# Kernel tuning notes

Measured on AMD Instinct MI355X. Metric: run time of the kernel, lower is better.

## Reference

```python
import jax, jax.numpy as jnp
import numpy as np

B, L, P, A, D = 64, 512, 64, 16, 512  # batch, seq_len, n_positions, n_actions, n_lstm


def setup_inputs() -> dict:
    key = jax.random.key(0)
    ks = jax.random.split(key, 6)
    F = P + A
    observations = jax.random.normal(ks[0], (B, L, P), jnp.float32)
    actions = jax.random.normal(ks[1], (B, L, A), jnp.float32)
    # xavier_normal init as in the torch module
    W_ci = jax.random.normal(ks[2], (F, D), jnp.float32) * np.float32(np.sqrt(2.0 / (F + D)))
    b_ci = jnp.zeros((D,), jnp.float32)
    R_ig = jax.random.normal(ks[3], (D, D), jnp.float32) * np.float32(np.sqrt(2.0 / (D + D)))
    b_ig = jnp.zeros((D,), jnp.float32)
    W_out = jax.random.normal(ks[4], (D, 1), jnp.float32) * np.float32(np.sqrt(2.0 / (D + 1)))
    b_out = jnp.zeros((1,), jnp.float32)
    return dict(observations=observations, actions=actions, W_ci=W_ci, b_ci=b_ci,
                R_ig=R_ig, b_ig=b_ig, W_out=W_out, b_out=b_out)


def reference(observations, actions, W_ci, b_ci, R_ig, b_ig, W_out, b_out):
    # Custom LSTM: forget gate = 1, output gate = 1, a_out = identity =>
    #   h_t = c_t = c_{t-1} + tanh(x_t @ W_ci + b_ci) * sigmoid(h_{t-1} @ R_ig + b_ig)
    x = jnp.concatenate([observations, actions], axis=-1)          # [B, L, F]
    ci = jnp.tanh(jnp.einsum('blf,fd->bld', x, W_ci) + b_ci)       # precompute cell input [B, L, D]
    ci_seq = jnp.swapaxes(ci, 0, 1)                                # [L, B, D] for scan
    h0 = jnp.zeros((x.shape[0], R_ig.shape[0]), x.dtype)

    def step(h, ci_t):
        ig = jax.nn.sigmoid(h @ R_ig + b_ig)
        h_new = h + ci_t * ig
        return h_new, h_new

    _, hs = jax.lax.scan(step, h0, ci_seq)                         # hs: [L, B, D]
    hs = jnp.swapaxes(hs, 0, 1)                                    # [B, L, D]
    return hs @ W_out + b_out                                      # [B, L, 1]
```

## Files before the change

### kernel.cpp

```cpp
#include <hip/hip_runtime.h>


#define B_  64
#define L_  512
#define P_  64
#define A_  16
#define D_  512
#define F_  80
#define CI_R 8

#define CI_BYTES   ((size_t)B_ * L_ * D_ * 2)
#define RP_BYTES   ((size_t)D_ * D_ * 2)
#define HBUF_UINTS (2 * B_ * 2 * 256)
#define PBANK      ((size_t)B_ * 2 * 256)
#define BATCH_CAP  4096

typedef _Float16 half2_t __attribute__((ext_vector_type(2)));
typedef unsigned int uintx4 __attribute__((ext_vector_type(4)));

__device__ __forceinline__ float dot2(unsigned int r, unsigned int h, float acc) {
    return __builtin_amdgcn_fdot2(__builtin_bit_cast(half2_t, h),
                                  __builtin_bit_cast(half2_t, r), acc, false);
}
__device__ __forceinline__ float dot4u(uintx4 r, uintx4 h, float acc) {
    acc = dot2(r.x, h.x, acc);
    acc = dot2(r.y, h.y, acc);
    acc = dot2(r.z, h.z, acc);
    acc = dot2(r.w, h.w, acc);
    return acc;
}
template<int CTRL>
__device__ __forceinline__ float dpp_mov(float v) {
    return __builtin_bit_cast(float, __builtin_amdgcn_update_dpp(
        0, __builtin_bit_cast(int, v), CTRL, 0xF, 0xF, true));
}

__device__ __forceinline__ unsigned int pk_f16(float a, float b) {
    return __builtin_bit_cast(unsigned int, __builtin_amdgcn_cvt_pkrtz(a, b));
}
__device__ __forceinline__ unsigned int ld_sc01(const unsigned int* p) {
    unsigned int v;
    asm volatile("global_load_dword %0, %1, off sc0 sc1\n\t"
                 "s_waitcnt vmcnt(0)" : "=v"(v) : "v"(p) : "memory");
    return v;
}
__device__ __forceinline__ void at_swap(unsigned int* p, unsigned int v) {
    asm volatile("global_atomic_swap %0, %1, off sc1" :: "v"(p), "v"(v) : "memory");
}
__device__ __forceinline__ int swz4(int i) {
    return ((i >> 3) << 3) | ((i + (i >> 3)) & 7);
}

__global__ __launch_bounds__(256) void prep_kernel(const float* __restrict__ R,
        unsigned int* __restrict__ Rp, unsigned int* __restrict__ hbuf,
        float* __restrict__ out) {
    int id = blockIdx.x * 256 + threadIdx.x;
    int dw = id & 3;
    int U = id >> 2;
    int tid_s = U & 511;
    int m  = (U >> 9) & 31;
    int qq = U >> 14;
    int w = tid_s >> 6, l = tid_s & 63, r = l >> 3, g = l & 7;
    int hh = m >> 4, j = (m >> 2) & 3, c = m & 3;
    int d  = qq * 256 + (w * 8 + r) * 4 + j;
    int k0 = hh * 256 + (g & 3) * 64 + (g >> 2) * 32 + c * 8 + 2 * dw;
    half2_t v;
    v.x = (_Float16)R[k0 * D_ + d];
    v.y = (_Float16)R[(k0 + 1) * D_ + d];
    Rp[id] = __builtin_bit_cast(unsigned int, v);
    if (id < HBUF_UINTS) hbuf[id] = 0u;
    if (id < B_ * L_) out[id] = 0.f;
}

__global__ __launch_bounds__(256) void ci_kernel(const float* __restrict__ obs,
                                                 const float* __restrict__ act,
                                                 const float* __restrict__ W,
                                                 const float* __restrict__ bci,
                                                 unsigned short* __restrict__ ci) {
    __shared__ float xs[CI_R][F_];
    int row0 = blockIdx.x * CI_R;
    int tid = threadIdx.x;
    for (int idx = tid; idx < CI_R * F_; idx += 256) {
        int r = idx / F_, f = idx % F_;
        float v = (f < P_) ? obs[(size_t)(row0 + r) * P_ + f]
                           : act[(size_t)(row0 + r) * A_ + (f - P_)];
        xs[r][f] = v;
    }
    __syncthreads();
    int d0 = tid, d1 = tid + 256;
    float a0[CI_R], a1[CI_R];
    #pragma unroll
    for (int r = 0; r < CI_R; ++r) { a0[r] = 0.f; a1[r] = 0.f; }
    for (int f = 0; f < F_; ++f) {
        float w0 = W[f * D_ + d0];
        float w1 = W[f * D_ + d1];
        #pragma unroll
        for (int r = 0; r < CI_R; ++r) {
            float xv = xs[r][f];
            a0[r] += xv * w0;
            a1[r] += xv * w1;
        }
    }
    float b0 = bci[d0], b1 = bci[d1];
    #pragma unroll
    for (int r = 0; r < CI_R; ++r) {
        float z0 = a0[r] + b0, z1 = a1[r] + b1;
        float e0 = __expf(-2.f * __builtin_fabsf(z0));
        float e1 = __expf(-2.f * __builtin_fabsf(z1));
        float m0 = (1.f - e0) * __builtin_amdgcn_rcpf(1.f + e0);
        float m1 = (1.f - e1) * __builtin_amdgcn_rcpf(1.f + e1);
        float t0 = z0 < 0.f ? -m0 : m0;
        float t1 = z1 < 0.f ? -m1 : m1;
        ci[(size_t)(row0 + r) * D_ + d0] = __builtin_bit_cast(unsigned short, (_Float16)t0);
        ci[(size_t)(row0 + r) * D_ + d1] = __builtin_bit_cast(unsigned short, (_Float16)t1);
    }
}

__global__ __launch_bounds__(512, 2)
__attribute__((amdgpu_waves_per_eu(2, 2)))
void scan_kernel(const unsigned int* __restrict__ Rp,
                 const unsigned short* __restrict__ ci,
                 const float* __restrict__ b_ig, const float* __restrict__ W_out,
                 const float* __restrict__ b_out, float* __restrict__ out,
                 unsigned int* __restrict__ hbuf)
{
    const int tid = threadIdx.x;
    const int bid = blockIdx.x;
    const int row = bid & 63;
    const int q   = bid >> 6;
    const int w = tid >> 6;
    const int l = tid & 63;
    const int r = l >> 3;
    const int g = l & 7;
    const int g3 = g & 3;

    __shared__ __align__(16) unsigned int hp2[128];
    __shared__ __align__(16) unsigned int hst[128];

    const uintx4* tb = (const uintx4*)Rp + (size_t)q * 16384 + tid;
    const int qx = q << 4;
    uintx4 rr[32];
    #pragma unroll
    for (int mm = 0; mm < 32; ++mm) rr[mm] = tb[(mm ^ qx) * 512];
    #pragma unroll
    for (int mm = 0; mm < 32; ++mm) asm volatile("" : "+v"(rr[mm]));

    const int dloc = (w * 8 + r) * 4 + g3;
    const int down = q * 256 + dloc;
    const float bg = b_ig[down];
    const float wo = W_out[down];
    const float bo = b_out[0];
    const unsigned short* cip = ci + (size_t)row * L_ * D_ + down;

    const int u_own = (w * 8 + r) * 2 + (g >> 1);
    const int wslot = swz4(u_own >> 2) * 4 + (u_own & 3);
    const int s_f = tid & 255;
    const int stslot = swz4(s_f >> 3) * 4 + ((s_f >> 1) & 3);
    const int ib = (g & 3) * 8 + (g >> 2) * 4;
    const int ri0 = swz4(ib + 0), ri1 = swz4(ib + 1);
    const int ri2 = swz4(ib + 2), ri3 = swz4(ib + 3);

    const unsigned int* rdbase = hbuf + ((size_t)row * 2 + (1 - q)) * 256 + s_f;
    unsigned int* wrbase = hbuf + ((size_t)row * 2 + q) * 256 + dloc;

    float hval = 0.f;
    __syncthreads();

    #pragma unroll 1
    for (int t = 0; t < L_; ++t) {
        unsigned short cu = cip[(size_t)t * D_];

        unsigned int vfetch = 0;
        const unsigned int* src = rdbase + (size_t)((t - 1) & 1) * PBANK;
        if (t > 0 && tid < 256) {
            asm volatile("global_load_dword %0, %1, off sc0 sc1"
                         : "=&v"(vfetch) : "v"(src) : "memory");
        }

        float p0 = 0.f, p1 = 0.f, p2 = 0.f, p3 = 0.f;

        if (t > 0) {
            const uintx4* hp4 = (const uintx4*)hp2;
            uintx4 h0 = hp4[ri0], h1 = hp4[ri1], h2 = hp4[ri2], h3 = hp4[ri3];
            p0 = dot4u(rr[0],  h0, p0); p0 = dot4u(rr[1],  h1, p0);
            p0 = dot4u(rr[2],  h2, p0); p0 = dot4u(rr[3],  h3, p0);
            p1 = dot4u(rr[4],  h0, p1); p1 = dot4u(rr[5],  h1, p1);
            p1 = dot4u(rr[6],  h2, p1); p1 = dot4u(rr[7],  h3, p1);
            p2 = dot4u(rr[8],  h0, p2); p2 = dot4u(rr[9],  h1, p2);
            p2 = dot4u(rr[10], h2, p2); p2 = dot4u(rr[11], h3, p2);
            p3 = dot4u(rr[12], h0, p3); p3 = dot4u(rr[13], h1, p3);
            p3 = dot4u(rr[14], h2, p3); p3 = dot4u(rr[15], h3, p3);
        }

        if (t > 0 && tid < 256) {
            asm volatile("s_waitcnt vmcnt(0)" : "+v"(vfetch) :: "memory");
            const unsigned int tt = (unsigned int)t;
            if ((vfetch & 0xffffu) != tt) {
                int it = 0;
                unsigned int a0, a1, a2;
                for (;;) {
                    asm volatile("global_load_dword %0, %1, off sc0 sc1"
                                 : "=&v"(a0) : "v"(src) : "memory");
                    __builtin_amdgcn_s_sleep(1);
                    asm volatile("global_load_dword %0, %1, off sc0 sc1"
                                 : "=&v"(a1) : "v"(src) : "memory");
                    __builtin_amdgcn_s_sleep(1);
                    asm volatile("global_load_dword %0, %1, off sc0 sc1"
                                 : "=&v"(a2) : "v"(src) : "memory");
                    asm volatile("s_waitcnt vmcnt(2)" ::: "memory");
                    if ((a0 & 0xffffu) == tt) {
                        vfetch = a0;
                        asm volatile("s_waitcnt vmcnt(0)" ::: "memory");
                        break;
                    }
                    asm volatile("s_waitcnt vmcnt(1)" ::: "memory");
                    if ((a1 & 0xffffu) == tt) {
                        vfetch = a1;
                        asm volatile("s_waitcnt vmcnt(0)" ::: "memory");
                        break;
                    }
                    asm volatile("s_waitcnt vmcnt(0)" ::: "memory");
                    if ((a2 & 0xffffu) == tt) { vfetch = a2; break; }
                    if (++it > BATCH_CAP) break;
                    __builtin_amdgcn_s_sleep(1);
                }
            }
            unsigned int vo = __builtin_bit_cast(unsigned int,
                                dpp_mov<0xB1>(__builtin_bit_cast(float, vfetch)));
            if ((tid & 1) == 0)
                hst[stslot] = (vfetch >> 16) | (vo & 0xffff0000u);
        }

        asm volatile("s_waitcnt lgkmcnt(0)" ::: "memory");
        __builtin_amdgcn_s_barrier();
        asm volatile("" ::: "memory");

        if (t > 0) {
            const uintx4* hs4 = (const uintx4*)hst;
            uintx4 h0 = hs4[ri0], h1 = hs4[ri1], h2 = hs4[ri2], h3 = hs4[ri3];
            p0 = dot4u(rr[16], h0, p0); p0 = dot4u(rr[17], h1, p0);
            p0 = dot4u(rr[18], h2, p0); p0 = dot4u(rr[19], h3, p0);
            p1 = dot4u(rr[20], h0, p1); p1 = dot4u(rr[21], h1, p1);
            p1 = dot4u(rr[22], h2, p1); p1 = dot4u(rr[23], h3, p1);
            p2 = dot4u(rr[24], h0, p2); p2 = dot4u(rr[25], h1, p2);
            p2 = dot4u(rr[26], h2, p2); p2 = dot4u(rr[27], h3, p2);
            p3 = dot4u(rr[28], h0, p3); p3 = dot4u(rr[29], h1, p3);
            p3 = dot4u(rr[30], h2, p3); p3 = dot4u(rr[31], h3, p3);
        }

        float s0 = p0 + dpp_mov<0x141>(p0);
        float s1 = p1 + dpp_mov<0x141>(p1);
        float s2 = p2 + dpp_mov<0x141>(p2);
        float s3 = p3 + dpp_mov<0x141>(p3);
        s0 = s0 + dpp_mov<0xB1>(s0);  s1 = s1 + dpp_mov<0xB1>(s1);
        s2 = s2 + dpp_mov<0xB1>(s2);  s3 = s3 + dpp_mov<0xB1>(s3);
        s0 = s0 + dpp_mov<0x4E>(s0);  s1 = s1 + dpp_mov<0x4E>(s1);
        s2 = s2 + dpp_mov<0x4E>(s2);  s3 = s3 + dpp_mov<0x4E>(s3);
        float z = ((g3 & 2) ? ((g3 & 1) ? s3 : s2)
                            : ((g3 & 1) ? s1 : s0)) + bg;

        float ig  = __builtin_amdgcn_rcpf(1.f + __expf(-z));
        float civ = (float)__builtin_bit_cast(_Float16, cu);
        hval += civ * ig;

        if (g < 4) {
            unsigned int hb = pk_f16(hval, hval) & 0xffffu;
            at_swap(wrbase + (size_t)(t & 1) * PBANK,
                    (hb << 16) | (unsigned int)(t + 1));
        }

        float nbh = dpp_mov<0xB1>(hval);
        if (g == 0 || g == 2) {
            hp2[wslot] = pk_f16(hval, nbh);
        }

        asm volatile("s_waitcnt lgkmcnt(0)" ::: "memory");
        __builtin_amdgcn_s_barrier();
        asm volatile("" ::: "memory");

        float po = (g < 4) ? hval * wo : 0.f;
        po += dpp_mov<0xB1>(po);
        po += dpp_mov<0x4E>(po);
        po += dpp_mov<0x141>(po);
        po += dpp_mov<0x140>(po);
        po += dpp_mov<0x142>(po);
        po += dpp_mov<0x143>(po);
        if (l == 63) {
            float addv = po + ((q == 0 && w == 0) ? bo : 0.f);
            atomicAdd(out + row * L_ + t, addv);
        }
    }
}

extern "C" void kernel_launch(void* const* d_in, const int* in_sizes, int n_in,
                              void* d_out, int out_size, void* d_ws, size_t ws_size,
                              hipStream_t stream) {
    const float* obs   = (const float*)d_in[0];
    const float* act   = (const float*)d_in[1];
    const float* W_ci  = (const float*)d_in[2];
    const float* b_ci  = (const float*)d_in[3];
    const float* R_ig  = (const float*)d_in[4];
    const float* b_ig  = (const float*)d_in[5];
    const float* W_out = (const float*)d_in[6];
    const float* b_out = (const float*)d_in[7];
    float* out = (float*)d_out;

    unsigned short* ci = (unsigned short*)d_ws;
    unsigned int* Rp   = (unsigned int*)((char*)d_ws + CI_BYTES);
    unsigned int* hbuf = (unsigned int*)((char*)d_ws + CI_BYTES + RP_BYTES);

    prep_kernel<<<512, 256, 0, stream>>>(R_ig, Rp, hbuf, out);
    ci_kernel<<<(B_ * L_) / CI_R, 256, 0, stream>>>(obs, act, W_ci, b_ci, ci);
    scan_kernel<<<B_ * 2, 512, 0, stream>>>(Rp, ci, b_ig, W_out, b_out, out, hbuf);
}
```

Measured before the change: 641.8 us.

## Fuse cell-input projection into scan kernel and drop separate ci kernel

Removes the standalone ci_kernel and its 32MB fp16 cell-input buffer. The prep kernel now packs W_ci and the concatenated inputs into fp16 pairs, and the scan kernel computes tanh(x·W_ci+b) per step with fdot2, using W_ci held in registers. This saves a kernel launch and the HBM round trip of the ci tensor. In exchange, the serial recurrence loop gains a 40-term dot product plus ten 16-byte loads per step, which may lengthen the critical path and raise register pressure.

```diff
diff --git a/kernel.cpp b/kernel.cpp
--- a/kernel.cpp
+++ b/kernel.cpp
@@ -7,10 +7,12 @@
 #define A_  16
 #define D_  512
 #define F_  80
-#define CI_R 8
-
-#define CI_BYTES   ((size_t)B_ * L_ * D_ * 2)
+
+#define XP_UINTS   (B_ * L_ * 40)
+#define XP_BYTES   ((size_t)XP_UINTS * 4)
 #define RP_BYTES   ((size_t)D_ * D_ * 2)
+#define WP_UINTS   (2 * 512 * 40)
+#define WP_BYTES   ((size_t)WP_UINTS * 4)
 #define HBUF_UINTS (2 * B_ * 2 * 256)
 #define PBANK      ((size_t)B_ * 2 * 256)
 #define BATCH_CAP  4096
@@ -38,12 +40,6 @@
 __device__ __forceinline__ unsigned int pk_f16(float a, float b) {
     return __builtin_bit_cast(unsigned int, __builtin_amdgcn_cvt_pkrtz(a, b));
 }
-__device__ __forceinline__ unsigned int ld_sc01(const unsigned int* p) {
-    unsigned int v;
-    asm volatile("global_load_dword %0, %1, off sc0 sc1\n\t"
-                 "s_waitcnt vmcnt(0)" : "=v"(v) : "v"(p) : "memory");
-    return v;
-}
 __device__ __forceinline__ void at_swap(unsigned int* p, unsigned int v) {
     asm volatile("global_atomic_swap %0, %1, off sc1" :: "v"(p), "v"(v) : "memory");
 }
@@ -52,74 +48,60 @@
 }
 
 __global__ __launch_bounds__(256) void prep_kernel(const float* __restrict__ R,
-        unsigned int* __restrict__ Rp, unsigned int* __restrict__ hbuf,
-        float* __restrict__ out) {
-    int id = blockIdx.x * 256 + threadIdx.x;
-    int dw = id & 3;
-    int U = id >> 2;
-    int tid_s = U & 511;
-    int m  = (U >> 9) & 31;
-    int qq = U >> 14;
-    int w = tid_s >> 6, l = tid_s & 63, r = l >> 3, g = l & 7;
-    int hh = m >> 4, j = (m >> 2) & 3, c = m & 3;
-    int d  = qq * 256 + (w * 8 + r) * 4 + j;
-    int k0 = hh * 256 + (g & 3) * 64 + (g >> 2) * 32 + c * 8 + 2 * dw;
-    half2_t v;
-    v.x = (_Float16)R[k0 * D_ + d];
-    v.y = (_Float16)R[(k0 + 1) * D_ + d];
-    Rp[id] = __builtin_bit_cast(unsigned int, v);
-    if (id < HBUF_UINTS) hbuf[id] = 0u;
-    if (id < B_ * L_) out[id] = 0.f;
-}
-
-__global__ __launch_bounds__(256) void ci_kernel(const float* __restrict__ obs,
-                                                 const float* __restrict__ act,
-                                                 const float* __restrict__ W,
-                                                 const float* __restrict__ bci,
-                                                 unsigned short* __restrict__ ci) {
-    __shared__ float xs[CI_R][F_];
-    int row0 = blockIdx.x * CI_R;
-    int tid = threadIdx.x;
-    for (int idx = tid; idx < CI_R * F_; idx += 256) {
-        int r = idx / F_, f = idx % F_;
-        float v = (f < P_) ? obs[(size_t)(row0 + r) * P_ + f]
-                           : act[(size_t)(row0 + r) * A_ + (f - P_)];
-        xs[r][f] = v;
-    }
-    __syncthreads();
-    int d0 = tid, d1 = tid + 256;
-    float a0[CI_R], a1[CI_R];
-    #pragma unroll
-    for (int r = 0; r < CI_R; ++r) { a0[r] = 0.f; a1[r] = 0.f; }
-    for (int f = 0; f < F_; ++f) {
-        float w0 = W[f * D_ + d0];
-        float w1 = W[f * D_ + d1];
-        #pragma unroll
-        for (int r = 0; r < CI_R; ++r) {
-            float xv = xs[r][f];
-            a0[r] += xv * w0;
-            a1[r] += xv * w1;
-        }
-    }
-    float b0 = bci[d0], b1 = bci[d1];
-    #pragma unroll
-    for (int r = 0; r < CI_R; ++r) {
-        float z0 = a0[r] + b0, z1 = a1[r] + b1;
-        float e0 = __expf(-2.f * __builtin_fabsf(z0));
-        float e1 = __expf(-2.f * __builtin_fabsf(z1));
-        float m0 = (1.f - e0) * __builtin_amdgcn_rcpf(1.f + e0);
-        float m1 = (1.f - e1) * __builtin_amdgcn_rcpf(1.f + e1);
-        float t0 = z0 < 0.f ? -m0 : m0;
-        float t1 = z1 < 0.f ? -m1 : m1;
-        ci[(size_t)(row0 + r) * D_ + d0] = __builtin_bit_cast(unsigned short, (_Float16)t0);
-        ci[(size_t)(row0 + r) * D_ + d1] = __builtin_bit_cast(unsigned short, (_Float16)t1);
+        const float* __restrict__ Wci, const float* __restrict__ obs,
+        const float* __restrict__ act, unsigned int* __restrict__ Rp,
+        unsigned int* __restrict__ Wp, unsigned int* __restrict__ xp,
+        unsigned int* __restrict__ hbuf, float* __restrict__ out) {
+    int blk = blockIdx.x;
+    if (blk < 512) {
+        int id = blk * 256 + threadIdx.x;
+        int dw = id & 3;
+        int U = id >> 2;
+        int tid_s = U & 511;
+        int m  = (U >> 9) & 31;
+        int qq = U >> 14;
+        int w = tid_s >> 6, l = tid_s & 63, r = l >> 3, g = l & 7;
+        int hh = m >> 4, j = (m >> 2) & 3, c = m & 3;
+        int d  = qq * 256 + (w * 8 + r) * 4 + j;
+        int k0 = hh * 256 + (g & 3) * 64 + (g >> 2) * 32 + c * 8 + 2 * dw;
+        half2_t v;
+        v.x = (_Float16)R[k0 * D_ + d];
+        v.y = (_Float16)R[(k0 + 1) * D_ + d];
+        Rp[id] = __builtin_bit_cast(unsigned int, v);
+        if (id < WP_UINTS) {
+            int i2 = id % 40, u2 = id / 40;
+            int q2 = u2 >> 9, t2 = u2 & 511;
+            int w2 = t2 >> 6, l2 = t2 & 63, r2 = l2 >> 3, g2 = l2 & 7;
+            int down2 = q2 * 256 + (w2 * 8 + r2) * 4 + (g2 & 3);
+            Wp[id] = pk_f16(Wci[(2 * i2) * D_ + down2],
+                            Wci[(2 * i2 + 1) * D_ + down2]);
+        }
+        if (id < HBUF_UINTS) hbuf[id] = 0u;
+        if (id < B_ * L_) out[id] = 0.f;
+    } else {
+        int id = (blk - 512) * 256 + threadIdx.x;
+        if (id < XP_UINTS) {
+            int i = id % 40, u = id / 40;
+            int t = u & 511, row = u >> 9;
+            float x0, x1;
+            if (i < 32) {
+                const float* ob = obs + ((size_t)row * L_ + t) * P_;
+                x0 = ob[2 * i]; x1 = ob[2 * i + 1];
+            } else {
+                const float* ac = act + ((size_t)row * L_ + t) * A_;
+                x0 = ac[2 * (i - 32)]; x1 = ac[2 * (i - 32) + 1];
+            }
+            xp[id] = pk_f16(x0, x1);
+        }
     }
 }
 
 __global__ __launch_bounds__(512, 2)
 __attribute__((amdgpu_waves_per_eu(2, 2)))
 void scan_kernel(const unsigned int* __restrict__ Rp,
-                 const unsigned short* __restrict__ ci,
+                 const unsigned int* __restrict__ Wp,
+                 const unsigned int* __restrict__ xp,
+                 const float* __restrict__ b_ci,
                  const float* __restrict__ b_ig, const float* __restrict__ W_out,
                  const float* __restrict__ b_out, float* __restrict__ out,
                  unsigned int* __restrict__ hbuf)
@@ -150,7 +132,16 @@
     const float bg = b_ig[down];
     const float wo = W_out[down];
     const float bo = b_out[0];
-    const unsigned short* cip = ci + (size_t)row * L_ * D_ + down;
+    const float bci = b_ci[down];
+
+    const uintx4* wpt = (const uintx4*)(Wp + ((size_t)q * 512 + tid) * 40);
+    uintx4 wv[10];
+    #pragma unroll
+    for (int i = 0; i < 10; ++i) wv[i] = wpt[i];
+    #pragma unroll
+    for (int i = 0; i < 10; ++i) asm volatile("" : "+v"(wv[i]));
+
+    const uintx4* xpt = (const uintx4*)(xp + (size_t)row * L_ * 40);
 
     const int u_own = (w * 8 + r) * 2 + (g >> 1);
     const int wslot = swz4(u_own >> 2) * 4 + (u_own & 3);
@@ -168,7 +159,11 @@
 
     #pragma unroll 1
     for (int t = 0; t < L_; ++t) {
-        unsigned short cu = cip[(size_t)t * D_];
+        uintx4 xv0 = xpt[t * 10 + 0], xv1 = xpt[t * 10 + 1];
+        uintx4 xv2 = xpt[t * 10 + 2], xv3 = xpt[t * 10 + 3];
+        uintx4 xv4 = xpt[t * 10 + 4], xv5 = xpt[t * 10 + 5];
+        uintx4 xv6 = xpt[t * 10 + 6], xv7 = xpt[t * 10 + 7];
+        uintx4 xv8 = xpt[t * 10 + 8], xv9 = xpt[t * 10 + 9];
 
         unsigned int vfetch = 0;
         const unsigned int* src = rdbase + (size_t)((t - 1) & 1) * PBANK;
@@ -191,6 +186,16 @@
             p3 = dot4u(rr[12], h0, p3); p3 = dot4u(rr[13], h1, p3);
             p3 = dot4u(rr[14], h2, p3); p3 = dot4u(rr[15], h3, p3);
         }
+
+        float zci = bci;
+        zci = dot4u(wv[0], xv0, zci); zci = dot4u(wv[1], xv1, zci);
+        zci = dot4u(wv[2], xv2, zci); zci = dot4u(wv[3], xv3, zci);
+        zci = dot4u(wv[4], xv4, zci); zci = dot4u(wv[5], xv5, zci);
+        zci = dot4u(wv[6], xv6, zci); zci = dot4u(wv[7], xv7, zci);
+        zci = dot4u(wv[8], xv8, zci); zci = dot4u(wv[9], xv9, zci);
+        float eci = __expf(-2.f * __builtin_fabsf(zci));
+        float mci = (1.f - eci) * __builtin_amdgcn_rcpf(1.f + eci);
+        float civ = zci < 0.f ? -mci : mci;
 
         if (t > 0 && tid < 256) {
             asm volatile("s_waitcnt vmcnt(0)" : "+v"(vfetch) :: "memory");
@@ -259,8 +264,7 @@
         float z = ((g3 & 2) ? ((g3 & 1) ? s3 : s2)
                             : ((g3 & 1) ? s1 : s0)) + bg;
 
-        float ig  = __builtin_amdgcn_rcpf(1.f + __expf(-z));
-        float civ = (float)__builtin_bit_cast(_Float16, cu);
+        float ig = __builtin_amdgcn_rcpf(1.f + __expf(-z));
         hval += civ * ig;
 
         if (g < 4) {
@@ -305,11 +309,12 @@
     const float* b_out = (const float*)d_in[7];
     float* out = (float*)d_out;
 
-    unsigned short* ci = (unsigned short*)d_ws;
-    unsigned int* Rp   = (unsigned int*)((char*)d_ws + CI_BYTES);
-    unsigned int* hbuf = (unsigned int*)((char*)d_ws + CI_BYTES + RP_BYTES);
-
-    prep_kernel<<<512, 256, 0, stream>>>(R_ig, Rp, hbuf, out);
-    ci_kernel<<<(B_ * L_) / CI_R, 256, 0, stream>>>(obs, act, W_ci, b_ci, ci);
-    scan_kernel<<<B_ * 2, 512, 0, stream>>>(Rp, ci, b_ig, W_out, b_out, out, hbuf);
-}
+    unsigned int* xp   = (unsigned int*)d_ws;
+    unsigned int* Rp   = (unsigned int*)((char*)d_ws + XP_BYTES);
+    unsigned int* Wp   = (unsigned int*)((char*)d_ws + XP_BYTES + RP_BYTES);
+    unsigned int* hbuf = (unsigned int*)((char*)d_ws + XP_BYTES + RP_BYTES + WP_BYTES);
+
+    prep_kernel<<<512 + (XP_UINTS + 255) / 256, 256, 0, stream>>>(
+        R_ig, W_ci, obs, act, Rp, Wp, xp, hbuf, out);
+    scan_kernel<<<B_ * 2, 512, 0, stream>>>(Rp, Wp, xp, b_ci, b_ig, W_out, b_out, out, hbuf);
+}
```

New measurement: 773.1 us. 1.2x slower.
